# Kernel optimization log

Hardware: AMD Instinct MI355X
Metric: run time of the kernel (lower is better)

The kernel has to match this reference:

```python
import jax, jax.numpy as jnp
import numpy as np

B, T, D, H = 4, 2048, 1024, 16
Dh = D // H  # 64


def setup_inputs() -> dict:
    key = jax.random.key(0)
    ks = jax.random.split(key, 12)
    s = 1.0 / np.sqrt(D)
    return {
        "q": jax.random.normal(ks[0], (B, T, D), jnp.float32),
        "k": jax.random.normal(ks[1], (B, T, D), jnp.float32),
        "v": jax.random.normal(ks[2], (B, T, D), jnp.float32),
        "Wq": jax.random.normal(ks[3], (D, D), jnp.float32) * s,
        "bq": jnp.zeros((D,), jnp.float32),
        "Wk": jax.random.normal(ks[4], (D, D), jnp.float32) * s,
        "bk": jnp.zeros((D,), jnp.float32),
        "Wv": jax.random.normal(ks[5], (Dh, D), jnp.float32) * s,
        "bv": jnp.zeros((Dh,), jnp.float32),
        "Wo": jax.random.normal(ks[6], (D, D), jnp.float32) * s,
        "bo": jnp.zeros((D,), jnp.float32),
    }


def reference(q, k, v, Wq, bq, Wk, bk, Wv, bv, Wo, bo):
    # Projections (torch Linear: y = x @ W.T + b)
    Q = (q @ Wq.T + bq).reshape(B, T, H, Dh)   # [B,T,H,Dh]
    K = (k @ Wk.T + bk).reshape(B, T, H, Dh)   # [B,T,H,Dh]
    Vs = v @ Wv.T + bv                         # [B,T,Dh] shared across heads
    scale = 1.0 / np.sqrt(Dh).astype(np.float32)
    scores = jnp.einsum('bqhd,bkhd->bhqk', Q, K) * scale  # [B,H,T,T]
    attn = jax.nn.softmax(scores, axis=-1)
    # shared-V: broadcast V over heads
    out = jnp.einsum('bhqk,bkd->bqhd', attn, Vs)  # [B,T,H,Dh]
    out = out.reshape(B, T, D)
    y = out @ Wo.T + bo                           # [B,T,D]
    return y, attn.mean(axis=1)                   # per-head-averaged attention
```

## Files before the change

### kernel.cpp

```cpp
#include <hip/hip_runtime.h>
#include <cstdint>
#include <cstddef>

typedef __attribute__((ext_vector_type(8))) _Float16 half8;
typedef __attribute__((ext_vector_type(4))) _Float16 half4;
typedef __attribute__((ext_vector_type(4))) float f32x4;

#define DEV static __device__ __forceinline__
#define AS1(p) (const __attribute__((address_space(1))) void*)(p)
#define AS3(p) (__attribute__((address_space(3))) void*)(p)

#define LDS_BARRIER() asm volatile("s_waitcnt lgkmcnt(0)\n\ts_barrier" ::: "memory")

DEV half8 cvt8(const float* p) {
    f32x4 a = *(const f32x4*)p;
    f32x4 b = *(const f32x4*)(p + 4);
    half8 o;
    o[0] = (_Float16)a[0]; o[1] = (_Float16)a[1];
    o[2] = (_Float16)a[2]; o[3] = (_Float16)a[3];
    o[4] = (_Float16)b[0]; o[5] = (_Float16)b[1];
    o[6] = (_Float16)b[2]; o[7] = (_Float16)b[3];
    return o;
}

__global__ __launch_bounds__(256)
void cvt5_kernel(const float* __restrict__ q, _Float16* __restrict__ oq,
                 const float* __restrict__ k, _Float16* __restrict__ ok,
                 const float* __restrict__ wq, _Float16* __restrict__ owq,
                 const float* __restrict__ wk, _Float16* __restrict__ owk,
                 const float* __restrict__ wo, _Float16* __restrict__ owo)
{
    const int NQ = 1048576, NW = 131072;
    const int total = 2 * NQ + 3 * NW;
    int i = blockIdx.x * 256 + threadIdx.x;
    int stride = gridDim.x * 256;
    for (; i < total; i += stride) {
        if (i < NQ)            ((half8*)oq)[i] = cvt8(q + (size_t)i * 8);
        else if (i < 2 * NQ)   ((half8*)ok)[i - NQ] = cvt8(k + (size_t)(i - NQ) * 8);
        else {
            int j = i - 2 * NQ;
            if (j < NW)        ((half8*)owq)[j] = cvt8(wq + (size_t)j * 8);
            else if (j < 2*NW) ((half8*)owk)[j - NW] = cvt8(wk + (size_t)(j - NW) * 8);
            else               ((half8*)owo)[j - 2*NW] = cvt8(wo + (size_t)(j - 2*NW) * 8);
        }
    }
}

__global__ __launch_bounds__(256)
void combine_kernel(const _Float16* __restrict__ a, const _Float16* __restrict__ b,
                    float* __restrict__ out, int n8)
{
    int i = blockIdx.x * 256 + threadIdx.x;
    int stride = gridDim.x * 256;
    for (; i < n8; i += stride) {
        half8 x = ((const half8*)a)[i];
        half8 y = ((const half8*)b)[i];
        f32x4 o0, o1;
#pragma unroll
        for (int j = 0; j < 4; j++) o0[j] = ((float)x[j] + (float)y[j]) * 0.0625f;
#pragma unroll
        for (int j = 0; j < 4; j++) o1[j] = ((float)x[j + 4] + (float)y[j + 4]) * 0.0625f;
        *(f32x4*)(out + (size_t)i * 8) = o0;
        *(f32x4*)(out + (size_t)i * 8 + 4) = o1;
    }
}

#define GEMM_BODY(A, B, bias, scale, Cout)                                        \
    __shared__ half8 As[2][512];                                                  \
    __shared__ half8 Bs[2][512];                                                  \
    const int tid = threadIdx.x, l = tid & 63, w = tid >> 6;                      \
    const int lr = l & 15, lh = l >> 4;                                           \
    const int wm0 = (w >> 1) * 64, wn0 = (w & 1) * 64;                            \
    const int bm0 = blockIdx.x * 128, bn0 = blockIdx.y * 128;                     \
    const int nsteps = K >> 5;                                                    \
    f32x4 acc[4][4] = {};                                                         \
    STAGE(0, 0);                                                                  \
    __syncthreads();                                                              \
    for (int t = 0; t < nsteps; t++) {                                            \
        int cur = t & 1;                                                          \
        if (t + 1 < nsteps) STAGE(cur ^ 1, t + 1);                                \
        half8 a[4], b[4];                                                         \
        _Pragma("unroll")                                                         \
        for (int m = 0; m < 4; m++) a[m] = As[cur][lh * 128 + wm0 + m * 16 + lr]; \
        _Pragma("unroll")                                                         \
        for (int n = 0; n < 4; n++) b[n] = Bs[cur][lh * 128 + wn0 + n * 16 + lr]; \
        _Pragma("unroll")                                                         \
        for (int m = 0; m < 4; m++)                                               \
            _Pragma("unroll")                                                     \
            for (int n = 0; n < 4; n++)                                           \
                acc[m][n] = __builtin_amdgcn_mfma_f32_16x16x32_f16(a[m], b[n], acc[m][n], 0, 0, 0); \
        __syncthreads();                                                          \
    }                                                                             \
    _Pragma("unroll")                                                             \
    for (int m = 0; m < 4; m++)                                                   \
        _Pragma("unroll")                                                         \
        for (int n = 0; n < 4; n++) {                                             \
            int row0 = bm0 + wm0 + m * 16 + lh * 4;                               \
            int col = bn0 + wn0 + n * 16 + lr;                                    \
            float bv = bias[col];                                                 \
            _Pragma("unroll")                                                     \
            for (int j = 0; j < 4; j++) {                                         \
                float val = (acc[m][n][j] + bv) * scale;                          \
                int row = row0 + j;                                               \
                if constexpr (OUT_F16)                                            \
                    ((_Float16*)Cout)[(size_t)row * N + col] = (_Float16)val;     \
                else                                                              \
                    ((float*)Cout)[(size_t)row * N + col] = val;                  \
            }                                                                     \
        }

#define STAGE(buf, t) do {                                                        \
        int k0 = (t) << 5;                                                        \
        _Pragma("unroll")                                                         \
        for (int q2 = 0; q2 < 2; q2++) {                                          \
            int r = q2 * 64 + l;                                                  \
            __builtin_amdgcn_global_load_lds(                                     \
                AS1(A + (size_t)(bm0 + r) * K + k0 + w * 8),                      \
                AS3(&As[buf][w * 128 + q2 * 64]), 16, 0, 0);                      \
            __builtin_amdgcn_global_load_lds(                                     \
                AS1(B + (size_t)(bn0 + r) * K + k0 + w * 8),                      \
                AS3(&Bs[buf][w * 128 + q2 * 64]), 16, 0, 0);                      \
        }                                                                         \
    } while (0)

template<bool OUT_F16>
__global__ __launch_bounds__(256, 2)
void gemm16(const _Float16* __restrict__ A, const _Float16* __restrict__ B,
            const float* __restrict__ bias, float scale, void* __restrict__ Cout,
            int M, int N, int K)
{
    GEMM_BODY(A, B, bias, scale, Cout)
}

template<bool OUT_F16>
__global__ __launch_bounds__(256, 2)
void gemm16_dual(const _Float16* __restrict__ A0, const _Float16* __restrict__ B0,
                 const float* __restrict__ bias0, float scale0, void* __restrict__ C0,
                 const _Float16* __restrict__ A1, const _Float16* __restrict__ B1,
                 const float* __restrict__ bias1, float scale1, void* __restrict__ C1,
                 int M, int N, int K)
{
    const _Float16* A = blockIdx.z ? A1 : A0;
    const _Float16* B = blockIdx.z ? B1 : B0;
    const float* bias = blockIdx.z ? bias1 : bias0;
    float scale = blockIdx.z ? scale1 : scale0;
    void* Cout = blockIdx.z ? C1 : C0;
    GEMM_BODY(A, B, bias, scale, Cout)
}
#undef STAGE

template<int BM, int BN, int WR, int WC>
__global__ __launch_bounds__(256, 2)
void gemm_vp(const float* __restrict__ Aptr, const float* __restrict__ Bw,
             const float* __restrict__ bias, _Float16* __restrict__ Cout, int M, int N, int K)
{
    constexpr int BK = 32;
    constexpr int WM = BM / WR, WN = BN / WC;
    constexpr int MF = WM / 16, NF = WN / 16;
    constexpr int LDT = 40;
    __shared__ _Float16 Asl[BM][LDT];
    __shared__ _Float16 Bsl[BN][LDT];

    const int tid = threadIdx.x;
    const int l = tid & 63;
    const int w = tid >> 6;
    const int wr = w / WC, wc = w % WC;
    const int lr = l & 15, lh = l >> 4;
    const int bm0 = blockIdx.y * BM, bn0 = blockIdx.x * BN;

    f32x4 acc[MF][NF] = {};

    for (int k0 = 0; k0 < K; k0 += BK) {
        __syncthreads();
        for (int c = tid; c < BM * 4; c += 256) {
            int row = c >> 2, c8 = (c & 3) << 3;
            *(half8*)&Asl[row][c8] = cvt8(Aptr + (size_t)(bm0 + row) * K + k0 + c8);
        }
        for (int c = tid; c < BN * 4; c += 256) {
            int row = c >> 2, c8 = (c & 3) << 3;
            *(half8*)&Bsl[row][c8] = cvt8(Bw + (size_t)(bn0 + row) * K + k0 + c8);
        }
        __syncthreads();

        half8 a[MF], b[NF];
#pragma unroll
        for (int m = 0; m < MF; m++)
            a[m] = *(const half8*)&Asl[wr * WM + m * 16 + lr][lh * 8];
#pragma unroll
        for (int n = 0; n < NF; n++)
            b[n] = *(const half8*)&Bsl[wc * WN + n * 16 + lr][lh * 8];
#pragma unroll
        for (int m = 0; m < MF; m++)
#pragma unroll
            for (int n = 0; n < NF; n++)
                acc[m][n] = __builtin_amdgcn_mfma_f32_16x16x32_f16(a[m], b[n], acc[m][n], 0, 0, 0);
    }

#pragma unroll
    for (int m = 0; m < MF; m++)
#pragma unroll
        for (int n = 0; n < NF; n++) {
            int row0 = bm0 + wr * WM + m * 16 + lh * 4;
            int col = bn0 + wc * WN + n * 16 + lr;
            float bv = bias[col];
#pragma unroll
            for (int j = 0; j < 4; j++) {
                float val = acc[m][n][j] + bv;
                int row = row0 + j;
                int bi = row >> 11, t = row & 2047;
                Cout[(((size_t)(bi * 64 + col)) << 11) + t] = (_Float16)val;
            }
        }
}

#define LK(dst, kt) do {                                                          \
        const _Float16* kp_ = Kb + (size_t)((kt) * 32) * 1024;                    \
        _Pragma("unroll")                                                         \
        for (int kfr_ = 0; kfr_ < 2; kfr_++)                                      \
            _Pragma("unroll")                                                     \
            for (int dk_ = 0; dk_ < 2; dk_++)                                     \
                dst[kfr_][dk_] = *(const half8*)(kp_ + (size_t)(kfr_ * 16 + lr) * 1024 \
                                                 + ch + dk_ * 32 + lh * 8);       \
    } while (0)

__global__ __launch_bounds__(512, 4)
void stats_kernel(const _Float16* __restrict__ Qh, const _Float16* __restrict__ Kh,
                  float* __restrict__ slp)
{
    const int blk = blockIdx.x;
    const int b = blk & 3;
    const int hg = (blk >> 2) & 1;
    const int q0 = (blk >> 3) << 5;
    const int tid = threadIdx.x;
    const int l = tid & 63, w = tid >> 6;
    const int lr = l & 15, lh = l >> 4;
    const int ch = (hg * 8 + w) * 64;

    const size_t base = (size_t)b * 2048 * 1024;
    const _Float16* Qb = Qh + base;
    const _Float16* Kb = Kh + base;

    half8 qf[2][2];
#pragma unroll
    for (int m = 0; m < 2; m++)
#pragma unroll
        for (int dk = 0; dk < 2; dk++)
            qf[m][dk] = *(const half8*)(Qb + (size_t)(q0 + m * 16 + lr) * 1024
                                        + ch + dk * 32 + lh * 8);

    float sl[2][4] = {};
    half8 ka[2][2], kb2[2][2];

#define SBODY(KF) do {                                                            \
        f32x4 sc[2][2] = {};                                                      \
        _Pragma("unroll")                                                         \
        for (int m = 0; m < 2; m++)                                               \
            _Pragma("unroll")                                                     \
            for (int kfr = 0; kfr < 2; kfr++)                                     \
                _Pragma("unroll")                                                 \
                for (int dk = 0; dk < 2; dk++)                                    \
                    sc[m][kfr] = __builtin_amdgcn_mfma_f32_16x16x32_f16(          \
                        qf[m][dk], KF[kfr][dk], sc[m][kfr], 0, 0, 0);             \
        _Pragma("unroll")                                                         \
        for (int m = 0; m < 2; m++)                                               \
            _Pragma("unroll")                                                     \
            for (int j = 0; j < 4; j++)                                           \
                sl[m][j] += __builtin_amdgcn_exp2f(sc[m][0][j])                   \
                          + __builtin_amdgcn_exp2f(sc[m][1][j]);                  \
    } while (0)

    LK(ka, 0);
    for (int kt = 0; kt < 64; kt += 2) {
        LK(kb2, kt + 1);
        SBODY(ka);
        LK(ka, kt + 2 < 64 ? kt + 2 : 63);
        SBODY(kb2);
    }
#undef SBODY

#pragma unroll
    for (int m = 0; m < 2; m++)
#pragma unroll
        for (int j = 0; j < 4; j++) {
            float s = sl[m][j];
#pragma unroll
            for (int d = 1; d < 16; d <<= 1)
                s += __shfl_xor(s, d, 64);
            if (lr == 0)
                slp[(size_t)(b * 16 + hg * 8 + w) * 2048 + q0 + m * 16 + lh * 4 + j] = s;
        }
}

__global__ __launch_bounds__(512, 4)
void emit_kernel(const _Float16* __restrict__ Qh, const _Float16* __restrict__ Kh,
                 const _Float16* __restrict__ VT, const float* __restrict__ slp,
                 _Float16* __restrict__ attnp, _Float16* __restrict__ Op)
{
    const int blk = blockIdx.x;
    const int b = blk & 3;
    const int hg = (blk >> 2) & 1;
    const int q0 = (blk >> 3) << 5;
    const int tid = threadIdx.x;
    const int l = tid & 63, w = tid >> 6;
    const int lr = l & 15, lh = l >> 4;
    const int ch = (hg * 8 + w) * 64;

    __shared__ __align__(16) _Float16 Pld[2][8][32][40];

    const size_t base = (size_t)b * 2048 * 1024;
    const _Float16* Qb = Qh + base;
    const _Float16* Kb = Kh + base;

    half8 qf[2][2];
#pragma unroll
    for (int m = 0; m < 2; m++)
#pragma unroll
        for (int dk = 0; dk < 2; dk++)
            qf[m][dk] = *(const half8*)(Qb + (size_t)(q0 + m * 16 + lr) * 1024
                                        + ch + dk * 32 + lh * 8);

    float rinv[2];
    {
        const float* sr = slp + (size_t)(b * 16 + hg * 8 + w) * 2048 + q0;
#pragma unroll
        for (int m = 0; m < 2; m++)
            rinv[m] = 1.0f / sr[m * 16 + lr];
    }

    f32x4 oacc[2][4] = {};
    half8 ka[2][2], kb2[2][2];

#define EBODY(KF, KT, P) do {                                                     \
        const int krow = (KT) * 32;                                               \
        f32x4 sc[2][2] = {};                                                      \
        _Pragma("unroll")                                                         \
        for (int m = 0; m < 2; m++)                                               \
            _Pragma("unroll")                                                     \
            for (int kfr = 0; kfr < 2; kfr++)                                     \
                _Pragma("unroll")                                                 \
                for (int dk = 0; dk < 2; dk++)                                    \
                    sc[m][kfr] = __builtin_amdgcn_mfma_f32_16x16x32_f16(          \
                        KF[kfr][dk], qf[m][dk], sc[m][kfr], 0, 0, 0);             \
        _Pragma("unroll")                                                         \
        for (int m = 0; m < 2; m++)                                               \
            _Pragma("unroll")                                                     \
            for (int kfr = 0; kfr < 2; kfr++) {                                   \
                half4 pk4;                                                        \
                _Pragma("unroll")                                                 \
                for (int j = 0; j < 4; j++)                                       \
                    pk4[j] = (_Float16)(__builtin_amdgcn_exp2f(sc[m][kfr][j])     \
                                        * rinv[m]);                               \
                *(half4*)&Pld[P][w][m * 16 + lr][kfr * 16 + lh * 4] = pk4;        \
            }                                                                     \
        half8 vf[4], pa[2];                                                       \
        _Pragma("unroll")                                                         \
        for (int dv = 0; dv < 4; dv++)                                            \
            vf[dv] = *(const half8*)(VT + (((size_t)(b * 64 + dv * 16 + lr)) << 11) + krow + lh * 8); \
        _Pragma("unroll")                                                         \
        for (int m = 0; m < 2; m++)                                               \
            pa[m] = *(const half8*)&Pld[P][w][m * 16 + lr][lh * 8];               \
        _Pragma("unroll")                                                         \
        for (int m = 0; m < 2; m++)                                               \
            _Pragma("unroll")                                                     \
            for (int dv = 0; dv < 4; dv++)                                        \
                oacc[m][dv] = __builtin_amdgcn_mfma_f32_16x16x32_f16(             \
                    pa[m], vf[dv], oacc[m][dv], 0, 0, 0);                         \
        LDS_BARRIER();                                                            \
        {                                                                         \
            int r = tid >> 4, c2 = (tid & 15) * 2;                                \
            float s0 = 0.f, s1 = 0.f;                                             \
            _Pragma("unroll")                                                     \
            for (int ww = 0; ww < 8; ww++) {                                      \
                union { uint32_t u; _Float16 h[2]; } pv;                          \
                pv.u = *(const uint32_t*)&Pld[P][ww][r][c2];                      \
                s0 += (float)pv.h[0]; s1 += (float)pv.h[1];                       \
            }                                                                     \
            union { _Float16 h[2]; uint32_t u; } pk;                              \
            pk.h[0] = (_Float16)s0; pk.h[1] = (_Float16)s1;                       \
            __builtin_nontemporal_store(pk.u, (uint32_t*)(attnp                   \
                + (size_t)hg * 16777216 + (((size_t)(b * 2048 + q0 + r)) << 11)   \
                + krow + c2));                                                    \
        }                                                                         \
    } while (0)

    LK(ka, 0);
    for (int i = 0; i < 64; i += 2) {
        LK(kb2, i + 1);
        EBODY(ka, i, 0);
        LK(ka, i + 2 < 64 ? i + 2 : 63);
        EBODY(kb2, i + 1, 1);
    }
#undef EBODY

    _Float16* op = Op + base;
#pragma unroll
    for (int m = 0; m < 2; m++)
#pragma unroll
        for (int dv = 0; dv < 4; dv++)
#pragma unroll
            for (int j = 0; j < 4; j++) {
                int row = q0 + m * 16 + lh * 4 + j;
                int col = ch + dv * 16 + lr;
                op[(size_t)row * 1024 + col] = (_Float16)oacc[m][dv][j];
            }
}

extern "C" void kernel_launch(void* const* d_in, const int* in_sizes, int n_in,
                              void* d_out, int out_size, void* d_ws, size_t ws_size,
                              hipStream_t stream)
{
    const float* q  = (const float*)d_in[0];
    const float* k  = (const float*)d_in[1];
    const float* v  = (const float*)d_in[2];
    const float* Wq = (const float*)d_in[3];
    const float* bq = (const float*)d_in[4];
    const float* Wk = (const float*)d_in[5];
    const float* bk = (const float*)d_in[6];
    const float* Wv = (const float*)d_in[7];
    const float* bv = (const float*)d_in[8];
    const float* Wo = (const float*)d_in[9];
    const float* bo = (const float*)d_in[10];

    float* y = (float*)d_out;
    float* attn_mean = y + (size_t)4 * 2048 * 1024;

    uint8_t* ws = (uint8_t*)d_ws;
    _Float16* Qh  = (_Float16*)(ws);
    _Float16* Kh  = (_Float16*)(ws + 16777216);
    _Float16* VT  = (_Float16*)(ws + 33554432);
    _Float16* Wqc = (_Float16*)(ws + 34603008);
    _Float16* Wkc = (_Float16*)(ws + 36700160);
    _Float16* Woc = (_Float16*)(ws + 38797312);
    _Float16* qc  = (_Float16*)(ws + 40894464);
    _Float16* kc  = (_Float16*)(ws + 57671680);
    _Float16* Op  = qc;
    _Float16* attnp = (_Float16*)(ws + 74448896);
    float*    slp = (float*)(ws + 34603008);

    const float QS = 0.125f * 1.44269504088896340736f;

    cvt5_kernel<<<dim3(2048), dim3(256), 0, stream>>>(q, qc, k, kc, Wq, Wqc, Wk, Wkc, Wo, Woc);

    gemm16_dual<true><<<dim3(64, 8, 2), dim3(256), 0, stream>>>(
        qc, Wqc, bq, QS, Qh, kc, Wkc, bk, 1.0f, Kh, 8192, 1024, 1024);
    gemm_vp<128, 64, 4, 1><<<dim3(1, 64), dim3(256), 0, stream>>>(v, Wv, bv, VT, 8192, 64, 1024);

    stats_kernel<<<dim3(512), dim3(512), 0, stream>>>(Qh, Kh, slp);
    emit_kernel<<<dim3(512), dim3(512), 0, stream>>>(Qh, Kh, VT, slp, attnp, Op);

    combine_kernel<<<dim3(2048), dim3(256), 0, stream>>>(
        attnp, attnp + (size_t)16777216, attn_mean, 2097152);

    gemm16<false><<<dim3(64, 8), dim3(256), 0, stream>>>(Op, Woc, bo, 1.0f, y, 8192, 1024, 1024);
}
```

Measured before the change: 566.3 us.

## Fuse head-mean reduction into emit kernel with 16-wave blocks covering all heads

The emit kernel now uses 1024-thread blocks where each of 16 waves handles one head for a 16-row query tile. The mean over all 16 heads is then reduced in LDS and written directly as fp32 attn_mean. This removes the two fp16 half-sum buffers and the separate combine kernel, cutting a large round trip of global memory traffic. In exchange each wave processes fewer query rows, so K and V fragments are reused less. The V projection launch also changes its tile configuration.

```diff
diff --git a/kernel.cpp b/kernel.cpp
--- a/kernel.cpp
+++ b/kernel.cpp
@@ -43,25 +43,6 @@
             else if (j < 2*NW) ((half8*)owk)[j - NW] = cvt8(wk + (size_t)(j - NW) * 8);
             else               ((half8*)owo)[j - 2*NW] = cvt8(wo + (size_t)(j - 2*NW) * 8);
         }
-    }
-}
-
-__global__ __launch_bounds__(256)
-void combine_kernel(const _Float16* __restrict__ a, const _Float16* __restrict__ b,
-                    float* __restrict__ out, int n8)
-{
-    int i = blockIdx.x * 256 + threadIdx.x;
-    int stride = gridDim.x * 256;
-    for (; i < n8; i += stride) {
-        half8 x = ((const half8*)a)[i];
-        half8 y = ((const half8*)b)[i];
-        f32x4 o0, o1;
-#pragma unroll
-        for (int j = 0; j < 4; j++) o0[j] = ((float)x[j] + (float)y[j]) * 0.0625f;
-#pragma unroll
-        for (int j = 0; j < 4; j++) o1[j] = ((float)x[j + 4] + (float)y[j + 4]) * 0.0625f;
-        *(f32x4*)(out + (size_t)i * 8) = o0;
-        *(f32x4*)(out + (size_t)i * 8 + 4) = o1;
     }
 }
 
@@ -291,95 +272,75 @@
         }
 }
 
-__global__ __launch_bounds__(512, 4)
-void emit_kernel(const _Float16* __restrict__ Qh, const _Float16* __restrict__ Kh,
-                 const _Float16* __restrict__ VT, const float* __restrict__ slp,
-                 _Float16* __restrict__ attnp, _Float16* __restrict__ Op)
+__global__ __launch_bounds__(1024, 4)
+void emit16_kernel(const _Float16* __restrict__ Qh, const _Float16* __restrict__ Kh,
+                   const _Float16* __restrict__ VT, const float* __restrict__ slp,
+                   float* __restrict__ attn_mean, _Float16* __restrict__ Op)
 {
     const int blk = blockIdx.x;
     const int b = blk & 3;
-    const int hg = (blk >> 2) & 1;
-    const int q0 = (blk >> 3) << 5;
+    const int q0 = (blk >> 2) << 4;
     const int tid = threadIdx.x;
     const int l = tid & 63, w = tid >> 6;
     const int lr = l & 15, lh = l >> 4;
-    const int ch = (hg * 8 + w) * 64;
-
-    __shared__ __align__(16) _Float16 Pld[2][8][32][40];
+    const int ch = w * 64;
+
+    __shared__ __align__(16) _Float16 Pld[2][16][16][40];
 
     const size_t base = (size_t)b * 2048 * 1024;
     const _Float16* Qb = Qh + base;
     const _Float16* Kb = Kh + base;
 
-    half8 qf[2][2];
-#pragma unroll
-    for (int m = 0; m < 2; m++)
-#pragma unroll
-        for (int dk = 0; dk < 2; dk++)
-            qf[m][dk] = *(const half8*)(Qb + (size_t)(q0 + m * 16 + lr) * 1024
-                                        + ch + dk * 32 + lh * 8);
-
-    float rinv[2];
-    {
-        const float* sr = slp + (size_t)(b * 16 + hg * 8 + w) * 2048 + q0;
-#pragma unroll
-        for (int m = 0; m < 2; m++)
-            rinv[m] = 1.0f / sr[m * 16 + lr];
-    }
-
-    f32x4 oacc[2][4] = {};
+    half8 qf[2];
+#pragma unroll
+    for (int dk = 0; dk < 2; dk++)
+        qf[dk] = *(const half8*)(Qb + (size_t)(q0 + lr) * 1024 + ch + dk * 32 + lh * 8);
+
+    const float rinv = 1.0f / slp[(size_t)(b * 16 + w) * 2048 + q0 + lr];
+
+    f32x4 oacc[4] = {};
     half8 ka[2][2], kb2[2][2];
+
+    const int rq = tid >> 6;
+    const int rc = tid & 31;
+    const int rhf = (tid >> 5) & 1;
 
 #define EBODY(KF, KT, P) do {                                                     \
         const int krow = (KT) * 32;                                               \
-        f32x4 sc[2][2] = {};                                                      \
-        _Pragma("unroll")                                                         \
-        for (int m = 0; m < 2; m++)                                               \
-            _Pragma("unroll")                                                     \
-            for (int kfr = 0; kfr < 2; kfr++)                                     \
-                _Pragma("unroll")                                                 \
-                for (int dk = 0; dk < 2; dk++)                                    \
-                    sc[m][kfr] = __builtin_amdgcn_mfma_f32_16x16x32_f16(          \
-                        KF[kfr][dk], qf[m][dk], sc[m][kfr], 0, 0, 0);             \
-        _Pragma("unroll")                                                         \
-        for (int m = 0; m < 2; m++)                                               \
-            _Pragma("unroll")                                                     \
-            for (int kfr = 0; kfr < 2; kfr++) {                                   \
-                half4 pk4;                                                        \
-                _Pragma("unroll")                                                 \
-                for (int j = 0; j < 4; j++)                                       \
-                    pk4[j] = (_Float16)(__builtin_amdgcn_exp2f(sc[m][kfr][j])     \
-                                        * rinv[m]);                               \
-                *(half4*)&Pld[P][w][m * 16 + lr][kfr * 16 + lh * 4] = pk4;        \
-            }                                                                     \
-        half8 vf[4], pa[2];                                                       \
+        f32x4 sc[2] = {};                 \
+        _Pragma("unroll")                                                         \
+        for (int kfr = 0; kfr < 2; kfr++)                                         \
+            _Pragma("unroll")                                                     \
+            for (int dk = 0; dk < 2; dk++)                                        \
+                sc[kfr] = __builtin_amdgcn_mfma_f32_16x16x32_f16(                 \
+                    KF[kfr][dk], qf[dk], sc[kfr], 0, 0, 0);                       \
+        _Pragma("unroll")                                                         \
+        for (int kfr = 0; kfr < 2; kfr++) {                                       \
+            half4 pk4;                                                            \
+            _Pragma("unroll")                                                     \
+            for (int j = 0; j < 4; j++)                                           \
+                pk4[j] = (_Float16)(__builtin_amdgcn_exp2f(sc[kfr][j]) * rinv);   \
+            *(half4*)&Pld[P][w][lr][kfr * 16 + lh * 4] = pk4;                     \
+        }                                                                         \
+        half8 vf[4], pa;                                                          \
         _Pragma("unroll")                                                         \
         for (int dv = 0; dv < 4; dv++)                                            \
             vf[dv] = *(const half8*)(VT + (((size_t)(b * 64 + dv * 16 + lr)) << 11) + krow + lh * 8); \
-        _Pragma("unroll")                                                         \
-        for (int m = 0; m < 2; m++)                                               \
-            pa[m] = *(const half8*)&Pld[P][w][m * 16 + lr][lh * 8];               \
-        _Pragma("unroll")                                                         \
-        for (int m = 0; m < 2; m++)                                               \
-            _Pragma("unroll")                                                     \
-            for (int dv = 0; dv < 4; dv++)                                        \
-                oacc[m][dv] = __builtin_amdgcn_mfma_f32_16x16x32_f16(             \
-                    pa[m], vf[dv], oacc[m][dv], 0, 0, 0);                         \
+        pa = *(const half8*)&Pld[P][w][lr][lh * 8];                               \
+        _Pragma("unroll")                                                         \
+        for (int dv = 0; dv < 4; dv++)                                            \
+            oacc[dv] = __builtin_amdgcn_mfma_f32_16x16x32_f16(                    \
+                pa, vf[dv], oacc[dv], 0, 0, 0);                                   \
         LDS_BARRIER();                                                            \
         {                                                                         \
-            int r = tid >> 4, c2 = (tid & 15) * 2;                                \
-            float s0 = 0.f, s1 = 0.f;                                             \
-            _Pragma("unroll")                                                     \
-            for (int ww = 0; ww < 8; ww++) {                                      \
-                union { uint32_t u; _Float16 h[2]; } pv;                          \
-                pv.u = *(const uint32_t*)&Pld[P][ww][r][c2];                      \
-                s0 += (float)pv.h[0]; s1 += (float)pv.h[1];                       \
-            }                                                                     \
-            union { _Float16 h[2]; uint32_t u; } pk;                              \
-            pk.h[0] = (_Float16)s0; pk.h[1] = (_Float16)s1;                       \
-            __builtin_nontemporal_store(pk.u, (uint32_t*)(attnp                   \
-                + (size_t)hg * 16777216 + (((size_t)(b * 2048 + q0 + r)) << 11)   \
-                + krow + c2));                                                    \
+            float s = 0.f;                                                        \
+            _Pragma("unroll")                                                     \
+            for (int ww = 0; ww < 8; ww++)                                        \
+                s += (float)Pld[P][rhf * 8 + ww][rq][rc];                         \
+            s += __shfl_xor(s, 32, 64);                                           \
+            if (rhf == 0)                                                         \
+                __builtin_nontemporal_store(s * 0.0625f,                          \
+                    &attn_mean[(((size_t)(b * 2048 + q0 + rq)) << 11) + krow + rc]); \
         }                                                                         \
     } while (0)
 
@@ -394,15 +355,13 @@
 
     _Float16* op = Op + base;
 #pragma unroll
-    for (int m = 0; m < 2; m++)
-#pragma unroll
-        for (int dv = 0; dv < 4; dv++)
-#pragma unroll
-            for (int j = 0; j < 4; j++) {
-                int row = q0 + m * 16 + lh * 4 + j;
-                int col = ch + dv * 16 + lr;
-                op[(size_t)row * 1024 + col] = (_Float16)oacc[m][dv][j];
-            }
+    for (int dv = 0; dv < 4; dv++)
+#pragma unroll
+        for (int j = 0; j < 4; j++) {
+            int row = q0 + lh * 4 + j;
+            int col = ch + dv * 16 + lr;
+            op[(size_t)row * 1024 + col] = (_Float16)oacc[dv][j];
+        }
 }
 
 extern "C" void kernel_launch(void* const* d_in, const int* in_sizes, int n_in,
@@ -434,7 +393,6 @@
     _Float16* qc  = (_Float16*)(ws + 40894464);
     _Float16* kc  = (_Float16*)(ws + 57671680);
     _Float16* Op  = qc;
-    _Float16* attnp = (_Float16*)(ws + 74448896);
     float*    slp = (float*)(ws + 34603008);
 
     const float QS = 0.125f * 1.44269504088896340736f;
@@ -443,13 +401,10 @@
 
     gemm16_dual<true><<<dim3(64, 8, 2), dim3(256), 0, stream>>>(
         qc, Wqc, bq, QS, Qh, kc, Wkc, bk, 1.0f, Kh, 8192, 1024, 1024);
-    gemm_vp<128, 64, 4, 1><<<dim3(1, 64), dim3(256), 0, stream>>>(v, Wv, bv, VT, 8192, 64, 1024);
+    gemm_vp<64, 64, 2, 2><<<dim3(1, 128), dim3(256), 0, stream>>>(v, Wv, bv, VT, 8192, 64, 1024);
 
     stats_kernel<<<dim3(512), dim3(512), 0, stream>>>(Qh, Kh, slp);
-    emit_kernel<<<dim3(512), dim3(512), 0, stream>>>(Qh, Kh, VT, slp, attnp, Op);
-
-    combine_kernel<<<dim3(2048), dim3(256), 0, stream>>>(
-        attnp, attnp + (size_t)16777216, attn_mean, 2097152);
+    emit16_kernel<<<dim3(512), dim3(1024), 0, stream>>>(Qh, Kh, VT, slp, attn_mean, Op);
 
     gemm16<false><<<dim3(64, 8), dim3(256), 0, stream>>>(Op, Woc, bo, 1.0f, y, 8192, 1024, 1024);
 }
```

Result: slower. 721.0 us (+27.3%).

## Fuse softmax stats and emit into one attention kernel, add 4-group variant

Applied to the files above, without the earlier changes.

Merges the separate row-sum statistics kernel into the emit kernel, so each block recomputes the exp-sum pass in registers and no longer writes or reads the slp buffer or pays a second launch. Adds a 256-thread variant that splits heads into four groups, giving twice as many smaller blocks. That variant writes four partial attention-mean buffers and combines them in a new combine4 kernel; it is chosen only when the workspace is large enough. The V projection tiling also changes. The cost is a larger partial-attention write and read in the four-group path.

```diff
diff --git a/kernel.cpp b/kernel.cpp
--- a/kernel.cpp
+++ b/kernel.cpp
@@ -60,6 +60,29 @@
         for (int j = 0; j < 4; j++) o0[j] = ((float)x[j] + (float)y[j]) * 0.0625f;
 #pragma unroll
         for (int j = 0; j < 4; j++) o1[j] = ((float)x[j + 4] + (float)y[j + 4]) * 0.0625f;
+        *(f32x4*)(out + (size_t)i * 8) = o0;
+        *(f32x4*)(out + (size_t)i * 8 + 4) = o1;
+    }
+}
+
+__global__ __launch_bounds__(256)
+void combine4_kernel(const _Float16* __restrict__ p, float* __restrict__ out, int n8)
+{
+    const size_t PS = 16777216;
+    int i = blockIdx.x * 256 + threadIdx.x;
+    int stride = gridDim.x * 256;
+    for (; i < n8; i += stride) {
+        half8 x0 = ((const half8*)p)[i];
+        half8 x1 = ((const half8*)(p + PS))[i];
+        half8 x2 = ((const half8*)(p + 2 * PS))[i];
+        half8 x3 = ((const half8*)(p + 3 * PS))[i];
+        f32x4 o0, o1;
+#pragma unroll
+        for (int j = 0; j < 4; j++)
+            o0[j] = ((float)x0[j] + (float)x1[j] + (float)x2[j] + (float)x3[j]) * 0.0625f;
+#pragma unroll
+        for (int j = 0; j < 4; j++)
+            o1[j] = ((float)x0[j+4] + (float)x1[j+4] + (float)x2[j+4] + (float)x3[j+4]) * 0.0625f;
         *(f32x4*)(out + (size_t)i * 8) = o0;
         *(f32x4*)(out + (size_t)i * 8 + 4) = o1;
     }
@@ -223,33 +246,40 @@
                                                  + ch + dk_ * 32 + lh * 8);       \
     } while (0)
 
-__global__ __launch_bounds__(512, 4)
-void stats_kernel(const _Float16* __restrict__ Qh, const _Float16* __restrict__ Kh,
-                  float* __restrict__ slp)
-{
-    const int blk = blockIdx.x;
-    const int b = blk & 3;
-    const int hg = (blk >> 2) & 1;
-    const int q0 = (blk >> 3) << 5;
-    const int tid = threadIdx.x;
-    const int l = tid & 63, w = tid >> 6;
-    const int lr = l & 15, lh = l >> 4;
-    const int ch = (hg * 8 + w) * 64;
-
-    const size_t base = (size_t)b * 2048 * 1024;
-    const _Float16* Qb = Qh + base;
-    const _Float16* Kb = Kh + base;
-
-    half8 qf[2][2];
-#pragma unroll
-    for (int m = 0; m < 2; m++)
-#pragma unroll
-        for (int dk = 0; dk < 2; dk++)
-            qf[m][dk] = *(const half8*)(Qb + (size_t)(q0 + m * 16 + lr) * 1024
-                                        + ch + dk * 32 + lh * 8);
-
-    float sl[2][4] = {};
-    half8 ka[2][2], kb2[2][2];
+#define PHASE1_RINV()                                                             \
+    float sl[2][4] = {};                                                          \
+    {                                                                             \
+        half8 ka[2][2], kb2[2][2];                                                \
+        LK(ka, 0);                                                                \
+        for (int kt = 0; kt < 64; kt += 2) {                                      \
+            LK(kb2, kt + 1);                                                      \
+            SBODY(ka);                                                            \
+            LK(ka, kt + 2 < 64 ? kt + 2 : 63);                                    \
+            SBODY(kb2);                                                           \
+        }                                                                         \
+    }                                                                             \
+    _Pragma("unroll")                                                             \
+    for (int m = 0; m < 2; m++)                                                   \
+        _Pragma("unroll")                                                         \
+        for (int j = 0; j < 4; j++) {                                             \
+            float s = sl[m][j];                                                   \
+            _Pragma("unroll")                                                     \
+            for (int d = 1; d < 16; d <<= 1)                                      \
+                s += __shfl_xor(s, d, 64);                                        \
+            sl[m][j] = s;                                                         \
+        }                                                                         \
+    float rinv[2];                                                                \
+    _Pragma("unroll")                                                             \
+    for (int m = 0; m < 2; m++) {                                                 \
+        int src = (lr >> 2) << 4;                                                 \
+        float t0 = __shfl(sl[m][0], src, 64);                                     \
+        float t1 = __shfl(sl[m][1], src, 64);                                     \
+        float t2 = __shfl(sl[m][2], src, 64);                                     \
+        float t3 = __shfl(sl[m][3], src, 64);                                     \
+        int jj = lr & 3;                                                          \
+        float s = (jj == 0) ? t0 : (jj == 1) ? t1 : (jj == 2) ? t2 : t3;          \
+        rinv[m] = 1.0f / s;                                                       \
+    }
 
 #define SBODY(KF) do {                                                            \
         f32x4 sc[2][2] = {};                                                      \
@@ -269,68 +299,7 @@
                           + __builtin_amdgcn_exp2f(sc[m][1][j]);                  \
     } while (0)
 
-    LK(ka, 0);
-    for (int kt = 0; kt < 64; kt += 2) {
-        LK(kb2, kt + 1);
-        SBODY(ka);
-        LK(ka, kt + 2 < 64 ? kt + 2 : 63);
-        SBODY(kb2);
-    }
-#undef SBODY
-
-#pragma unroll
-    for (int m = 0; m < 2; m++)
-#pragma unroll
-        for (int j = 0; j < 4; j++) {
-            float s = sl[m][j];
-#pragma unroll
-            for (int d = 1; d < 16; d <<= 1)
-                s += __shfl_xor(s, d, 64);
-            if (lr == 0)
-                slp[(size_t)(b * 16 + hg * 8 + w) * 2048 + q0 + m * 16 + lh * 4 + j] = s;
-        }
-}
-
-__global__ __launch_bounds__(512, 4)
-void emit_kernel(const _Float16* __restrict__ Qh, const _Float16* __restrict__ Kh,
-                 const _Float16* __restrict__ VT, const float* __restrict__ slp,
-                 _Float16* __restrict__ attnp, _Float16* __restrict__ Op)
-{
-    const int blk = blockIdx.x;
-    const int b = blk & 3;
-    const int hg = (blk >> 2) & 1;
-    const int q0 = (blk >> 3) << 5;
-    const int tid = threadIdx.x;
-    const int l = tid & 63, w = tid >> 6;
-    const int lr = l & 15, lh = l >> 4;
-    const int ch = (hg * 8 + w) * 64;
-
-    __shared__ __align__(16) _Float16 Pld[2][8][32][40];
-
-    const size_t base = (size_t)b * 2048 * 1024;
-    const _Float16* Qb = Qh + base;
-    const _Float16* Kb = Kh + base;
-
-    half8 qf[2][2];
-#pragma unroll
-    for (int m = 0; m < 2; m++)
-#pragma unroll
-        for (int dk = 0; dk < 2; dk++)
-            qf[m][dk] = *(const half8*)(Qb + (size_t)(q0 + m * 16 + lr) * 1024
-                                        + ch + dk * 32 + lh * 8);
-
-    float rinv[2];
-    {
-        const float* sr = slp + (size_t)(b * 16 + hg * 8 + w) * 2048 + q0;
-#pragma unroll
-        for (int m = 0; m < 2; m++)
-            rinv[m] = 1.0f / sr[m * 16 + lr];
-    }
-
-    f32x4 oacc[2][4] = {};
-    half8 ka[2][2], kb2[2][2];
-
-#define EBODY(KF, KT, P) do {                                                     \
+#define EBODY_CORE(KF, KT, P, NW)                                                 \
         const int krow = (KT) * 32;                                               \
         f32x4 sc[2][2] = {};                                                      \
         _Pragma("unroll")                                                         \
@@ -365,7 +334,43 @@
             for (int dv = 0; dv < 4; dv++)                                        \
                 oacc[m][dv] = __builtin_amdgcn_mfma_f32_16x16x32_f16(             \
                     pa[m], vf[dv], oacc[m][dv], 0, 0, 0);                         \
-        LDS_BARRIER();                                                            \
+        LDS_BARRIER();
+
+__global__ __launch_bounds__(512, 4)
+void attn_fused(const _Float16* __restrict__ Qh, const _Float16* __restrict__ Kh,
+                const _Float16* __restrict__ VT, _Float16* __restrict__ attnp,
+                _Float16* __restrict__ Op)
+{
+    const int blk = blockIdx.x;
+    const int b = blk & 3;
+    const int hg = (blk >> 2) & 1;
+    const int q0 = (blk >> 3) << 5;
+    const int tid = threadIdx.x;
+    const int l = tid & 63, w = tid >> 6;
+    const int lr = l & 15, lh = l >> 4;
+    const int ch = (hg * 8 + w) * 64;
+
+    __shared__ __align__(16) _Float16 Pld[2][8][32][40];
+
+    const size_t base = (size_t)b * 2048 * 1024;
+    const _Float16* Qb = Qh + base;
+    const _Float16* Kb = Kh + base;
+
+    half8 qf[2][2];
+#pragma unroll
+    for (int m = 0; m < 2; m++)
+#pragma unroll
+        for (int dk = 0; dk < 2; dk++)
+            qf[m][dk] = *(const half8*)(Qb + (size_t)(q0 + m * 16 + lr) * 1024
+                                        + ch + dk * 32 + lh * 8);
+
+    PHASE1_RINV()
+
+    f32x4 oacc[2][4] = {};
+    half8 ka[2][2], kb2[2][2];
+
+#define EBODY(KF, KT, P) do {                                                     \
+        EBODY_CORE(KF, KT, P, 8)                                                  \
         {                                                                         \
             int r = tid >> 4, c2 = (tid & 15) * 2;                                \
             float s0 = 0.f, s1 = 0.f;                                             \
@@ -405,6 +410,82 @@
             }
 }
 
+__global__ __launch_bounds__(256, 4)
+void attn_fused4(const _Float16* __restrict__ Qh, const _Float16* __restrict__ Kh,
+                 const _Float16* __restrict__ VT, _Float16* __restrict__ attnp,
+                 _Float16* __restrict__ Op)
+{
+    const int blk = blockIdx.x;
+    const int b = blk & 3;
+    const int hq = (blk >> 2) & 3;
+    const int q0 = (blk >> 4) << 5;
+    const int tid = threadIdx.x;
+    const int l = tid & 63, w = tid >> 6;
+    const int lr = l & 15, lh = l >> 4;
+    const int ch = (hq * 4 + w) * 64;
+
+    __shared__ __align__(16) _Float16 Pld[2][4][32][40];
+
+    const size_t base = (size_t)b * 2048 * 1024;
+    const _Float16* Qb = Qh + base;
+    const _Float16* Kb = Kh + base;
+
+    half8 qf[2][2];
+#pragma unroll
+    for (int m = 0; m < 2; m++)
+#pragma unroll
+        for (int dk = 0; dk < 2; dk++)
+            qf[m][dk] = *(const half8*)(Qb + (size_t)(q0 + m * 16 + lr) * 1024
+                                        + ch + dk * 32 + lh * 8);
+
+    PHASE1_RINV()
+
+    f32x4 oacc[2][4] = {};
+    half8 ka[2][2], kb2[2][2];
+
+#define EBODY(KF, KT, P) do {                                                     \
+        EBODY_CORE(KF, KT, P, 4)                                                  \
+        {                                                                         \
+            int r = tid >> 3, c4 = (tid & 7) * 4;                                 \
+            float s0 = 0.f, s1 = 0.f, s2 = 0.f, s3 = 0.f;                         \
+            _Pragma("unroll")                                                     \
+            for (int ww = 0; ww < 4; ww++) {                                      \
+                union { uint64_t u; _Float16 h[4]; } pv;                          \
+                pv.u = *(const uint64_t*)&Pld[P][ww][r][c4];                      \
+                s0 += (float)pv.h[0]; s1 += (float)pv.h[1];                       \
+                s2 += (float)pv.h[2]; s3 += (float)pv.h[3];                       \
+            }                                                                     \
+            union { _Float16 h[4]; uint64_t u; } pk;                              \
+            pk.h[0] = (_Float16)s0; pk.h[1] = (_Float16)s1;                       \
+            pk.h[2] = (_Float16)s2; pk.h[3] = (_Float16)s3;                       \
+            __builtin_nontemporal_store(pk.u, (uint64_t*)(attnp                   \
+                + (size_t)hq * 16777216 + (((size_t)(b * 2048 + q0 + r)) << 11)   \
+                + krow + c4));                                                    \
+        }                                                                         \
+    } while (0)
+
+    LK(ka, 0);
+    for (int i = 0; i < 64; i += 2) {
+        LK(kb2, i + 1);
+        EBODY(ka, i, 0);
+        LK(ka, i + 2 < 64 ? i + 2 : 63);
+        EBODY(kb2, i + 1, 1);
+    }
+#undef EBODY
+
+    _Float16* op = Op + base;
+#pragma unroll
+    for (int m = 0; m < 2; m++)
+#pragma unroll
+        for (int dv = 0; dv < 4; dv++)
+#pragma unroll
+            for (int j = 0; j < 4; j++) {
+                int row = q0 + m * 16 + lh * 4 + j;
+                int col = ch + dv * 16 + lr;
+                op[(size_t)row * 1024 + col] = (_Float16)oacc[m][dv][j];
+            }
+}
+
 extern "C" void kernel_launch(void* const* d_in, const int* in_sizes, int n_in,
                               void* d_out, int out_size, void* d_ws, size_t ws_size,
                               hipStream_t stream)
@@ -435,7 +516,8 @@
     _Float16* kc  = (_Float16*)(ws + 57671680);
     _Float16* Op  = qc;
     _Float16* attnp = (_Float16*)(ws + 74448896);
-    float*    slp = (float*)(ws + 34603008);
+
+    const bool four = ws_size >= 208666624ull;
 
     const float QS = 0.125f * 1.44269504088896340736f;
 
@@ -443,13 +525,16 @@
 
     gemm16_dual<true><<<dim3(64, 8, 2), dim3(256), 0, stream>>>(
         qc, Wqc, bq, QS, Qh, kc, Wkc, bk, 1.0f, Kh, 8192, 1024, 1024);
-    gemm_vp<128, 64, 4, 1><<<dim3(1, 64), dim3(256), 0, stream>>>(v, Wv, bv, VT, 8192, 64, 1024);
-
-    stats_kernel<<<dim3(512), dim3(512), 0, stream>>>(Qh, Kh, slp);
-    emit_kernel<<<dim3(512), dim3(512), 0, stream>>>(Qh, Kh, VT, slp, attnp, Op);
-
-    combine_kernel<<<dim3(2048), dim3(256), 0, stream>>>(
-        attnp, attnp + (size_t)16777216, attn_mean, 2097152);
+    gemm_vp<64, 64, 2, 2><<<dim3(1, 128), dim3(256), 0, stream>>>(v, Wv, bv, VT, 8192, 64, 1024);
+
+    if (four) {
+        attn_fused4<<<dim3(1024), dim3(256), 0, stream>>>(Qh, Kh, VT, attnp, Op);
+        combine4_kernel<<<dim3(2048), dim3(256), 0, stream>>>(attnp, attn_mean, 2097152);
+    } else {
+        attn_fused<<<dim3(512), dim3(512), 0, stream>>>(Qh, Kh, VT, attnp, Op);
+        combine_kernel<<<dim3(2048), dim3(256), 0, stream>>>(
+            attnp, attnp + (size_t)16777216, attn_mean, 2097152);
+    }
 
     gemm16<false><<<dim3(64, 8), dim3(256), 0, stream>>>(Op, Woc, bo, 1.0f, y, 8192, 1024, 1024);
 }
```

Result: faster. 542.7 us (-4.2%).
